# Kernel tuning notes

Measured on AMD Instinct MI355X. Metric: run time of the kernel, lower is better.

Reference implementation:

```python
import jax, jax.numpy as jnp
import numpy as np

HEAD_SIZE = 64


def setup_inputs() -> dict:
    key = jax.random.key(0)
    kx, kq, kk, kv = jax.random.split(key, 4)
    B, L, D = 4, 4096, 1024
    scale = 1.0 / np.sqrt(D)
    x = jax.random.normal(kx, (B, L, D), dtype=jnp.float32)
    Wq = jax.random.normal(kq, (D, HEAD_SIZE), dtype=jnp.float32) * scale
    Wk = jax.random.normal(kk, (D, HEAD_SIZE), dtype=jnp.float32) * scale
    Wv = jax.random.normal(kv, (D, HEAD_SIZE), dtype=jnp.float32) * scale
    return {"x": x, "Wq": Wq, "Wk": Wk, "Wv": Wv}


def reference(x, Wq, Wk, Wv):
    B, L, D = x.shape
    H = Wq.shape[1]
    q = jnp.einsum('bld,dh->blh', x, Wq)  # [B,L,H]
    k = jnp.einsum('bld,dh->blh', x, Wk)
    v = jnp.einsum('bld,dh->blh', x, Wv)
    # full L x L score matrix, as in the original module
    scores = jnp.einsum('bqh,bkh->bqk', q, k) / jnp.sqrt(jnp.float32(H))
    causal = jnp.tril(jnp.ones((L, L), dtype=bool))
    scores = jnp.where(causal, scores, -jnp.inf)
    attn = jax.nn.softmax(scores, axis=-1)
    z = jnp.einsum('bqk,bkh->bqh', attn, v)  # [B,L,H]
    return z
```

## Files before the change

kernel.cpp:

```cpp
#include <hip/hip_runtime.h>
#include <stdint.h>

#define L_SEQ 4096
#define D_MODEL 1024
#define HEAD 64
#define KCH 512
#define MAXCH 8
#define NQT 32

typedef unsigned short u16;
typedef _Float16 f16;
typedef __attribute__((ext_vector_type(8))) f16 f16x8;
typedef __attribute__((ext_vector_type(2))) __fp16 fp16x2;
typedef __attribute__((ext_vector_type(4))) float f32x4;

static __device__ __forceinline__ u16 f16bits(float f) {
    union { f16 h; u16 u; } c; c.h = (f16)f; return c.u;
}
static __device__ __forceinline__ uint32_t pk16(float a, float b) {
    union { fp16x2 h; uint32_t u; } c;
    c.h = __builtin_amdgcn_cvt_pkrtz(a, b);
    return c.u;
}
static __device__ __forceinline__ f16x8 ld8h(const u16* p) { return *(const f16x8*)p; }

static __device__ __forceinline__ f32x4 mfma16h(f16x8 a, f16x8 b, f32x4 c) {
    return __builtin_amdgcn_mfma_f32_16x16x32_f16(a, b, c, 0, 0, 0);
}

static __device__ __forceinline__ void gload16(const u16* g, u16* l) {
    __builtin_amdgcn_global_load_lds(
        (const __attribute__((address_space(1))) void*)g,
        (__attribute__((address_space(3))) void*)l, 16, 0, 0);
}

static __device__ __forceinline__ int Sq(int qt) {
    int f = qt >> 2, r = qt & 3;
    return (f + 1) * (2 * f + r);
}

__global__ __launch_bounds__(256) void conv_w(
    const float* __restrict__ Wq, const float* __restrict__ Wk,
    const float* __restrict__ Wv, u16* __restrict__ Wt)
{
    __shared__ u16 tile[64][72];
    const float* W = (blockIdx.y == 0) ? Wq : (blockIdx.y == 1) ? Wk : Wv;
    const float sc = (blockIdx.y == 0) ? 0.18033688f : 1.0f;
    u16* dst = Wt + blockIdx.y * (HEAD * D_MODEL);
    const int k0 = blockIdx.x * 64, t = threadIdx.x;
    #pragma unroll
    for (int i = 0; i < 16; i++) {
        int idx = i * 256 + t;
        int kk = idx >> 6, h = idx & 63;
        tile[h][kk] = f16bits(W[(size_t)(k0 + kk) * HEAD + h] * sc);
    }
    __syncthreads();
    #pragma unroll
    for (int i = 0; i < 16; i++) {
        int idx = i * 256 + t;
        int h = idx >> 6, kk = idx & 63;
        dst[(size_t)h * D_MODEL + k0 + kk] = tile[h][kk];
    }
}

__global__ __launch_bounds__(256, 4) void qkv_proj(
    const float* __restrict__ x, const u16* __restrict__ Wt,
    u16* __restrict__ qb, u16* __restrict__ kb, u16* __restrict__ vTb)
{
    __shared__ __align__(16) u16 Wl[2 * 192 * 32];
    __shared__ __align__(16) u16 Xl[2 * 32 * 36];
#define WLX(dh,r,c) Wl[((dh)*192 + (r))*32 + (c)]
#define XLX(kh,r,c) Xl[((kh)*32  + (r))*36 + (c)]
#define CT(r,c)     Wl[(r)*200 + (c)]

    const int t = threadIdx.x;
    const int wv = t >> 6, lane = t & 63;
    const int ln16 = lane & 15, quad = lane >> 4;
    const int w3 = wv * 3;
    const int m0 = blockIdx.x * 32;

    f32x4 acc[2][3] = {};
    float4 xv0, xv1;
    f16x8 wreg[6];

    auto loadW = [&](int s) {
        const int k0 = s * 64;
        #pragma unroll
        for (int k2 = 0; k2 < 6; k2++) {
            int c = wv * 6 + k2;
            int dh = c & 1, g = c >> 1;
            wreg[k2] = ld8h(Wt + (size_t)(g * 16 + (lane >> 2)) * D_MODEL
                               + k0 + dh * 32 + (lane & 3) * 8);
        }
    };
    auto writeW = [&]() {
        #pragma unroll
        for (int k2 = 0; k2 < 6; k2++) {
            int c = wv * 6 + k2;
            int dh = c & 1, g = c >> 1;
            *(f16x8*)&WLX(dh, g * 16 + (lane >> 2), (lane & 3) * 8) = wreg[k2];
        }
    };
    auto loadx = [&](int s) {
        const int k0 = s * 64;
        int r0 = t >> 4, cs0 = (t & 15) * 4;
        xv0 = *(const float4*)&x[(size_t)(m0 + r0) * D_MODEL + k0 + cs0];
        int idx = 256 + t, r1 = idx >> 4, cs1 = (idx & 15) * 4;
        xv1 = *(const float4*)&x[(size_t)(m0 + r1) * D_MODEL + k0 + cs1];
    };
    auto packx = [&]() {
        int r0 = t >> 4, cs0 = (t & 15) * 4;
        uint2 p0; p0.x = pk16(xv0.x, xv0.y); p0.y = pk16(xv0.z, xv0.w);
        *(uint2*)&XLX(cs0 >> 5, r0, cs0 & 31) = p0;
        int idx = 256 + t, r1 = idx >> 4, cs1 = (idx & 15) * 4;
        uint2 p1; p1.x = pk16(xv1.x, xv1.y); p1.y = pk16(xv1.z, xv1.w);
        *(uint2*)&XLX(cs1 >> 5, r1, cs1 & 31) = p1;
    };

    loadW(0); loadx(0); writeW(); packx();
    for (int s = 0; s < 16; s++) {
        __syncthreads();
        if (s + 1 < 16) { loadW(s + 1); loadx(s + 1); }
        #pragma unroll
        for (int c = 0; c < 2; c++) {
            f16x8 xb0 = ld8h(&XLX(c, ln16, quad * 8));
            f16x8 xb1 = ld8h(&XLX(c, 16 + ln16, quad * 8));
            #pragma unroll
            for (int j = 0; j < 3; j++) {
                f16x8 af = ld8h(&WLX(c, (w3 + j) * 16 + ln16, quad * 8));
                acc[0][j] = mfma16h(af, xb0, acc[0][j]);
                acc[1][j] = mfma16h(af, xb1, acc[1][j]);
            }
        }
        __syncthreads();
        if (s + 1 < 16) { writeW(); packx(); }
    }

    __syncthreads();
    #pragma unroll
    for (int mt = 0; mt < 2; mt++) {
        #pragma unroll
        for (int j = 0; j < 3; j++) {
            int g0 = (w3 + j) * 16 + quad * 4;
            uint2 pk;
            pk.x = pk16(acc[mt][j][0], acc[mt][j][1]);
            pk.y = pk16(acc[mt][j][2], acc[mt][j][3]);
            *(uint2*)&CT(mt * 16 + ln16, g0) = pk;
        }
    }
    __syncthreads();
    {
        int m = t >> 3, hg = (t & 7) * 8;
        *(f16x8*)&qb[(size_t)(m0 + m) * HEAD + hg] = *(f16x8*)&CT(m, hg);
        *(f16x8*)&kb[(size_t)(m0 + m) * HEAD + hg] = *(f16x8*)&CT(m, 64 + hg);
        int h = t >> 2, mg = (t & 3) * 8;
        f16x8 vvv;
        #pragma unroll
        for (int jj = 0; jj < 8; jj++)
            ((u16*)&vvv)[jj] = CT(mg + jj, 128 + h);
        int bbt = m0 >> 12, l0 = m0 & 4095;
        *(f16x8*)&vTb[(size_t)(bbt * HEAD + h) * L_SEQ + l0 + mg] = vvv;
    }
#undef WLX
#undef XLX
#undef CT
}

__global__ __launch_bounds__(256, 4) void attn_chunk(
    const u16* __restrict__ qb, const u16* __restrict__ kb,
    const u16* __restrict__ vT, float* __restrict__ Opart, float* __restrict__ lpart,
    float* __restrict__ out)
{
    const int id = blockIdx.x;
    const int b = id & 3;
    int qt, ch;
    if (id < 480) {
        int fi = id >> 2;
        int acc = 0;
        qt = 31; ch = 0;
        #pragma unroll
        for (int k = 0; k < 32; k++) {
            int nf = (k + 1) >> 2;
            if (fi < acc + nf) { qt = k; ch = fi - acc; break; }
            acc += nf;
        }
    } else {
        int pi = (id - 480) >> 2;
        int m = pi & 7;
        qt = (pi < 8) ? (4 * m + 2) : (pi < 16) ? (4 * m + 1) : (4 * m);
        ch = m;
    }

    __shared__ __align__(16) u16 Kls[2 * 64 * 32];
    __shared__ __align__(16) u16 Vls[2 * 64 * 32];
    __shared__ __align__(16) u16 Pls[4 * 32 * 72];
#define KBX(dh,r,c) Kls[((dh)*64 + (r))*32 + (c)]
#define VBX(kh,r,c) Vls[((kh)*64 + (r))*32 + (c)]
#define PX(r,c)     Pls[((wv)*32 + (r))*72 + (c)]

    const int t = threadIdx.x, wv = t >> 6, lane = t & 63;
    const int ln16 = lane & 15, quad = lane >> 4;
    const int qmin = qt * 128 + wv * 32;
    const int nch = (qt + 4) >> 2;

    f16x8 qf[2][2];
    #pragma unroll
    for (int qn = 0; qn < 2; qn++) {
        const u16* qrp = qb + (size_t)(b * L_SEQ + qmin + qn * 16 + ln16) * HEAD + quad * 8;
        qf[qn][0] = ld8h(qrp); qf[qn][1] = ld8h(qrp + 32);
    }

    const u16* kbb = kb + (size_t)b * L_SEQ * HEAD;
    const u16* vbb = vT + (size_t)b * HEAD * L_SEQ;

    f32x4 o[2][4] = {};
    float lsum[2] = {0.f, 0.f};

    const int kv_lo = ch * KCH;
    const int kv_hi = min(kv_lo + KCH, qt * 128 + 128);
    const int nst = (kv_hi - kv_lo) >> 6;

    auto issueK = [&](int kv0) {
        #pragma unroll
        for (int k2 = 0; k2 < 2; k2++) {
            int c = wv * 2 + k2;
            int dh = c & 1, g = c >> 1;
            const u16* gp = kbb + (size_t)(kv0 + g * 16 + (lane >> 2)) * HEAD
                                + dh * 32 + (lane & 3) * 8;
            gload16(gp, &KBX(dh, g * 16 + (lane >> 2), (lane & 3) * 8));
        }
    };
    auto issueV = [&](int kv0) {
        #pragma unroll
        for (int k2 = 0; k2 < 2; k2++) {
            int c = wv * 2 + k2;
            int kh = c & 1, g = c >> 1;
            const u16* gp = vbb + (size_t)(g * 16 + (lane >> 2)) * L_SEQ
                                + kv0 + kh * 32 + (lane & 3) * 8;
            gload16(gp, &VBX(kh, g * 16 + (lane >> 2), (lane & 3) * 8));
        }
    };

    issueK(kv_lo); issueV(kv_lo);
    __syncthreads();

    for (int s = 0; s < nst; s++) {
        const int kv0 = kv_lo + s * 64;

        #pragma unroll
        for (int g = 0; g < 4; g++) {
            f16x8 ka0 = ld8h(&KBX(0, g * 16 + ln16, quad * 8));
            f16x8 ka1 = ld8h(&KBX(1, g * 16 + ln16, quad * 8));
            #pragma unroll
            for (int qn = 0; qn < 2; qn++) {
                f32x4 s2 = {};
                s2 = mfma16h(ka0, qf[qn][0], s2);
                s2 = mfma16h(ka1, qf[qn][1], s2);
                float p0, p1, p2, p3;
                if (kv0 + g * 16 + 15 <= qmin + qn * 16) {
                    p0 = __builtin_amdgcn_exp2f(s2[0]);
                    p1 = __builtin_amdgcn_exp2f(s2[1]);
                    p2 = __builtin_amdgcn_exp2f(s2[2]);
                    p3 = __builtin_amdgcn_exp2f(s2[3]);
                } else {
                    int q = qmin + qn * 16 + ln16;
                    int kv = kv0 + g * 16 + quad * 4;
                    p0 = (kv     <= q) ? __builtin_amdgcn_exp2f(s2[0]) : 0.f;
                    p1 = (kv + 1 <= q) ? __builtin_amdgcn_exp2f(s2[1]) : 0.f;
                    p2 = (kv + 2 <= q) ? __builtin_amdgcn_exp2f(s2[2]) : 0.f;
                    p3 = (kv + 3 <= q) ? __builtin_amdgcn_exp2f(s2[3]) : 0.f;
                }
                lsum[qn] += (p0 + p1) + (p2 + p3);
                uint2 pk; pk.x = pk16(p0, p1); pk.y = pk16(p2, p3);
                *(uint2*)&PX(qn * 16 + ln16, g * 16 + quad * 4) = pk;
            }
        }

        __syncthreads();
        if (s + 1 < nst) issueK(kv0 + 64);

        f16x8 pf[2][2];
        #pragma unroll
        for (int qn = 0; qn < 2; qn++) {
            pf[qn][0] = ld8h(&PX(qn * 16 + ln16, quad * 8));
            pf[qn][1] = ld8h(&PX(qn * 16 + ln16, 32 + quad * 8));
        }
        #pragma unroll
        for (int hg = 0; hg < 4; hg++) {
            f16x8 va0 = ld8h(&VBX(0, hg * 16 + ln16, quad * 8));
            f16x8 va1 = ld8h(&VBX(1, hg * 16 + ln16, quad * 8));
            #pragma unroll
            for (int qn = 0; qn < 2; qn++) {
                o[qn][hg] = mfma16h(va0, pf[qn][0], o[qn][hg]);
                o[qn][hg] = mfma16h(va1, pf[qn][1], o[qn][hg]);
            }
        }

        __syncthreads();
        if (s + 1 < nst) issueV(kv0 + 64);
    }

    #pragma unroll
    for (int qn = 0; qn < 2; qn++) {
        lsum[qn] += __shfl_xor(lsum[qn], 16);
        lsum[qn] += __shfl_xor(lsum[qn], 32);
    }

    if (nch == 1) {
        #pragma unroll
        for (int qn = 0; qn < 2; qn++) {
            float inv = 1.f / lsum[qn];
            int q = qmin + qn * 16 + ln16;
            #pragma unroll
            for (int hg = 0; hg < 4; hg++) {
                float4 r;
                r.x = o[qn][hg][0] * inv; r.y = o[qn][hg][1] * inv;
                r.z = o[qn][hg][2] * inv; r.w = o[qn][hg][3] * inv;
                *(float4*)&out[((size_t)(b * L_SEQ + q)) * HEAD + hg * 16 + quad * 4] = r;
            }
        }
        return;
    }

    const size_t base = (size_t)(b * 144 + Sq(qt) + ch);
    #pragma unroll
    for (int qn = 0; qn < 2; qn++) {
        int q_local = wv * 32 + qn * 16 + ln16;
        #pragma unroll
        for (int hg = 0; hg < 4; hg++)
            *(f32x4*)&Opart[base * 8192 + (size_t)q_local * 64 + hg * 16 + quad * 4] = o[qn][hg];
        if (quad == 0)
            lpart[base * 128 + q_local] = lsum[qn];
    }
#undef KBX
#undef VBX
#undef PX
}

__global__ __launch_bounds__(256) void merge_chunks(
    const float* __restrict__ Opart, const float* __restrict__ lpart,
    float* __restrict__ out)
{
    const int qt = blockIdx.x + 4, qseg = blockIdx.y, b = blockIdx.z;
    const int nch = (qt + 4) >> 2;
    const int t = threadIdx.x;
    const size_t obase = (size_t)(b * 144 + Sq(qt)) * 8192;
    const size_t lbase = (size_t)(b * 144 + Sq(qt)) * 128;
    #pragma unroll
    for (int i = 0; i < 2; i++) {
        int idx = i * 256 + t;
        int q = qseg * 32 + (idx >> 4), hg = (idx & 15) * 4;
        float L = 0.f, ax = 0.f, ay = 0.f, az = 0.f, aw = 0.f;
        #pragma unroll
        for (int c = 0; c < MAXCH; c++) {
            if (c < nch) {
                L += lpart[lbase + c * 128 + q];
                const float4 v = *(const float4*)&Opart[obase + (size_t)c * 8192 + q * 64 + hg];
                ax += v.x; ay += v.y; az += v.z; aw += v.w;
            }
        }
        float inv = 1.f / L;
        float4 r; r.x = ax * inv; r.y = ay * inv; r.z = az * inv; r.w = aw * inv;
        *(float4*)&out[((size_t)(b * L_SEQ + qt * 128 + q)) * HEAD + hg] = r;
    }
}

extern "C" void kernel_launch(void* const* d_in, const int* in_sizes, int n_in,
                              void* d_out, int out_size, void* d_ws, size_t ws_size,
                              hipStream_t stream) {
    const float* x  = (const float*)d_in[0];
    const float* Wq = (const float*)d_in[1];
    const float* Wk = (const float*)d_in[2];
    const float* Wv = (const float*)d_in[3];
    float* out = (float*)d_out;

    u16* ws16 = (u16*)d_ws;
    u16* Wt  = ws16;
    u16* qb  = Wt + 3 * HEAD * D_MODEL;
    u16* kb  = qb + 16384 * HEAD;
    u16* vTb = kb + 16384 * HEAD;
    float* Opart = (float*)(vTb + 16384 * HEAD);
    float* lpart = Opart + (size_t)4 * 144 * 8192;

    conv_w      <<<dim3(16, 3), 256, 0, stream>>>(Wq, Wk, Wv, Wt);
    qkv_proj    <<<dim3(512), 256, 0, stream>>>(x, Wt, qb, kb, vTb);
    attn_chunk  <<<dim3(576), 256, 0, stream>>>(qb, kb, vTb, Opart, lpart, out);
    merge_chunks<<<dim3(NQT - 4, 4, 4), 256, 0, stream>>>(Opart, lpart, out);
}
```

Before: 146.9 us.

## XOR-swizzle shared-memory tiles and double-buffer x prefetch two stages ahead

Applies an XOR swizzle to the 16-byte column chunks of the W, K and V shared-memory tiles, in both the projection and the attention kernels. This is meant to cut LDS bank conflicts on the row-strided MFMA operand reads. For K/V the swizzle is applied on the global-load address side of the direct-to-LDS loads. The projection kernel also keeps two sets of x registers and prefetches x two stages ahead so global latency is better hidden, at the cost of extra VGPRs.

```diff
diff --git a/kernel.cpp b/kernel.cpp
--- a/kernel.cpp
+++ b/kernel.cpp
@@ -78,9 +78,12 @@
     const int ln16 = lane & 15, quad = lane >> 4;
     const int w3 = wv * 3;
     const int m0 = blockIdx.x * 32;
+    const int r4 = lane >> 2, cl = lane & 3;
+    const int cswz = (cl ^ (r4 & 3)) * 8;
+    const int qsw = (quad ^ (ln16 & 3)) * 8;
 
     f32x4 acc[2][3] = {};
-    float4 xv0, xv1;
+    float4 xa0, xa1, xb0, xb1;
     f16x8 wreg[6];
 
     auto loadW = [&](int s) {
@@ -89,8 +92,8 @@
         for (int k2 = 0; k2 < 6; k2++) {
             int c = wv * 6 + k2;
             int dh = c & 1, g = c >> 1;
-            wreg[k2] = ld8h(Wt + (size_t)(g * 16 + (lane >> 2)) * D_MODEL
-                               + k0 + dh * 32 + (lane & 3) * 8);
+            wreg[k2] = ld8h(Wt + (size_t)(g * 16 + r4) * D_MODEL
+                               + k0 + dh * 32 + cl * 8);
         }
     };
     auto writeW = [&]() {
@@ -98,42 +101,62 @@
         for (int k2 = 0; k2 < 6; k2++) {
             int c = wv * 6 + k2;
             int dh = c & 1, g = c >> 1;
-            *(f16x8*)&WLX(dh, g * 16 + (lane >> 2), (lane & 3) * 8) = wreg[k2];
-        }
-    };
-    auto loadx = [&](int s) {
+            *(f16x8*)&WLX(dh, g * 16 + r4, cswz) = wreg[k2];
+        }
+    };
+    auto loadxAB = [&](int s, float4& v0, float4& v1) {
         const int k0 = s * 64;
-        int r0 = t >> 4, cs0 = (t & 15) * 4;
-        xv0 = *(const float4*)&x[(size_t)(m0 + r0) * D_MODEL + k0 + cs0];
-        int idx = 256 + t, r1 = idx >> 4, cs1 = (idx & 15) * 4;
-        xv1 = *(const float4*)&x[(size_t)(m0 + r1) * D_MODEL + k0 + cs1];
-    };
-    auto packx = [&]() {
-        int r0 = t >> 4, cs0 = (t & 15) * 4;
-        uint2 p0; p0.x = pk16(xv0.x, xv0.y); p0.y = pk16(xv0.z, xv0.w);
-        *(uint2*)&XLX(cs0 >> 5, r0, cs0 & 31) = p0;
-        int idx = 256 + t, r1 = idx >> 4, cs1 = (idx & 15) * 4;
-        uint2 p1; p1.x = pk16(xv1.x, xv1.y); p1.y = pk16(xv1.z, xv1.w);
-        *(uint2*)&XLX(cs1 >> 5, r1, cs1 & 31) = p1;
-    };
-
-    loadW(0); loadx(0); writeW(); packx();
-    for (int s = 0; s < 16; s++) {
-        __syncthreads();
-        if (s + 1 < 16) { loadW(s + 1); loadx(s + 1); }
+        int rr0 = t >> 4, cs0 = (t & 15) * 4;
+        v0 = *(const float4*)&x[(size_t)(m0 + rr0) * D_MODEL + k0 + cs0];
+        int idx = 256 + t, rr1 = idx >> 4, cs1 = (idx & 15) * 4;
+        v1 = *(const float4*)&x[(size_t)(m0 + rr1) * D_MODEL + k0 + cs1];
+    };
+    auto packxAB = [&](const float4& v0, const float4& v1) {
+        int rr0 = t >> 4, cs0 = (t & 15) * 4;
+        uint2 p0; p0.x = pk16(v0.x, v0.y); p0.y = pk16(v0.z, v0.w);
+        *(uint2*)&XLX(cs0 >> 5, rr0, cs0 & 31) = p0;
+        int idx = 256 + t, rr1 = idx >> 4, cs1 = (idx & 15) * 4;
+        uint2 p1; p1.x = pk16(v1.x, v1.y); p1.y = pk16(v1.z, v1.w);
+        *(uint2*)&XLX(cs1 >> 5, rr1, cs1 & 31) = p1;
+    };
+    auto mfmaBody = [&]() {
         #pragma unroll
         for (int c = 0; c < 2; c++) {
-            f16x8 xb0 = ld8h(&XLX(c, ln16, quad * 8));
-            f16x8 xb1 = ld8h(&XLX(c, 16 + ln16, quad * 8));
+            f16x8 xb_0 = ld8h(&XLX(c, ln16, quad * 8));
+            f16x8 xb_1 = ld8h(&XLX(c, 16 + ln16, quad * 8));
             #pragma unroll
             for (int j = 0; j < 3; j++) {
-                f16x8 af = ld8h(&WLX(c, (w3 + j) * 16 + ln16, quad * 8));
-                acc[0][j] = mfma16h(af, xb0, acc[0][j]);
-                acc[1][j] = mfma16h(af, xb1, acc[1][j]);
+                f16x8 af = ld8h(&WLX(c, (w3 + j) * 16 + ln16, qsw));
+                acc[0][j] = mfma16h(af, xb_0, acc[0][j]);
+                acc[1][j] = mfma16h(af, xb_1, acc[1][j]);
             }
         }
-        __syncthreads();
-        if (s + 1 < 16) { writeW(); packx(); }
+    };
+
+    loadW(0); loadxAB(0, xa0, xa1);
+    writeW(); packxAB(xa0, xa1);
+    loadxAB(1, xb0, xb1);
+
+    #pragma unroll 1
+    for (int sp = 0; sp < 8; sp++) {
+        {
+            int s = 2 * sp;
+            __syncthreads();
+            if (s + 1 < 16) loadW(s + 1);
+            if (s + 2 < 16) loadxAB(s + 2, xa0, xa1);
+            mfmaBody();
+            __syncthreads();
+            if (s + 1 < 16) { writeW(); packxAB(xb0, xb1); }
+        }
+        {
+            int s = 2 * sp + 1;
+            __syncthreads();
+            if (s + 1 < 16) loadW(s + 1);
+            if (s + 2 < 16) loadxAB(s + 2, xb0, xb1);
+            mfmaBody();
+            __syncthreads();
+            if (s + 1 < 16) { writeW(); packxAB(xa0, xa1); }
+        }
     }
 
     __syncthreads();
@@ -202,6 +225,9 @@
     const int ln16 = lane & 15, quad = lane >> 4;
     const int qmin = qt * 128 + wv * 32;
     const int nch = (qt + 4) >> 2;
+    const int r4 = lane >> 2, cl = lane & 3;
+    const int csw8 = ((cl ^ (r4 & 3))) * 8;
+    const int qsw = (quad ^ (ln16 & 3)) * 8;
 
     f16x8 qf[2][2];
     #pragma unroll
@@ -225,9 +251,9 @@
         for (int k2 = 0; k2 < 2; k2++) {
             int c = wv * 2 + k2;
             int dh = c & 1, g = c >> 1;
-            const u16* gp = kbb + (size_t)(kv0 + g * 16 + (lane >> 2)) * HEAD
-                                + dh * 32 + (lane & 3) * 8;
-            gload16(gp, &KBX(dh, g * 16 + (lane >> 2), (lane & 3) * 8));
+            const u16* gp = kbb + (size_t)(kv0 + g * 16 + r4) * HEAD
+                                + dh * 32 + csw8;
+            gload16(gp, &KBX(dh, g * 16 + r4, cl * 8));
         }
     };
     auto issueV = [&](int kv0) {
@@ -235,9 +261,9 @@
         for (int k2 = 0; k2 < 2; k2++) {
             int c = wv * 2 + k2;
             int kh = c & 1, g = c >> 1;
-            const u16* gp = vbb + (size_t)(g * 16 + (lane >> 2)) * L_SEQ
-                                + kv0 + kh * 32 + (lane & 3) * 8;
-            gload16(gp, &VBX(kh, g * 16 + (lane >> 2), (lane & 3) * 8));
+            const u16* gp = vbb + (size_t)(g * 16 + r4) * L_SEQ
+                                + kv0 + kh * 32 + csw8;
+            gload16(gp, &VBX(kh, g * 16 + r4, cl * 8));
         }
     };
 
@@ -249,8 +275,8 @@
 
         #pragma unroll
         for (int g = 0; g < 4; g++) {
-            f16x8 ka0 = ld8h(&KBX(0, g * 16 + ln16, quad * 8));
-            f16x8 ka1 = ld8h(&KBX(1, g * 16 + ln16, quad * 8));
+            f16x8 ka0 = ld8h(&KBX(0, g * 16 + ln16, qsw));
+            f16x8 ka1 = ld8h(&KBX(1, g * 16 + ln16, qsw));
             #pragma unroll
             for (int qn = 0; qn < 2; qn++) {
                 f32x4 s2 = {};
@@ -287,8 +313,8 @@
         }
         #pragma unroll
         for (int hg = 0; hg < 4; hg++) {
-            f16x8 va0 = ld8h(&VBX(0, hg * 16 + ln16, quad * 8));
-            f16x8 va1 = ld8h(&VBX(1, hg * 16 + ln16, quad * 8));
+            f16x8 va0 = ld8h(&VBX(0, hg * 16 + ln16, qsw));
+            f16x8 va1 = ld8h(&VBX(1, hg * 16 + ln16, qsw));
             #pragma unroll
             for (int qn = 0; qn < 2; qn++) {
                 o[qn][hg] = mfma16h(va0, pf[qn][0], o[qn][hg]);
```

Result: no change. 147.6 us (+0.5%).

## Double K-step tile depth in projection and attention kernels to halve barriers

Applied to the files above, without the earlier changes.

The QKV projection now stages 128 reduction columns of W and x per iteration instead of 64, so it runs 8 iterations instead of 16. The attention kernel now loads 128 keys/values per stage and processes them as two 64-wide halves, computing the first half's PV product before the barrier. The aim is to cut the number of block barriers and loop iterations and to give more independent work between global loads. In exchange, LDS use and register use roughly double, so launch bounds drop to 2 blocks per CU for the projection and 3 for attention, which lowers occupancy.

```diff
diff --git a/kernel.cpp b/kernel.cpp
--- a/kernel.cpp
+++ b/kernel.cpp
@@ -63,12 +63,12 @@
     }
 }
 
-__global__ __launch_bounds__(256, 4) void qkv_proj(
+__global__ __launch_bounds__(256, 2) void qkv_proj(
     const float* __restrict__ x, const u16* __restrict__ Wt,
     u16* __restrict__ qb, u16* __restrict__ kb, u16* __restrict__ vTb)
 {
-    __shared__ __align__(16) u16 Wl[2 * 192 * 32];
-    __shared__ __align__(16) u16 Xl[2 * 32 * 36];
+    __shared__ __align__(16) u16 Wl[4 * 192 * 32];
+    __shared__ __align__(16) u16 Xl[4 * 32 * 36];
 #define WLX(dh,r,c) Wl[((dh)*192 + (r))*32 + (c)]
 #define XLX(kh,r,c) Xl[((kh)*32  + (r))*36 + (c)]
 #define CT(r,c)     Wl[(r)*200 + (c)]
@@ -78,51 +78,59 @@
     const int ln16 = lane & 15, quad = lane >> 4;
     const int w3 = wv * 3;
     const int m0 = blockIdx.x * 32;
+    const int r4 = lane >> 2, cl8 = (lane & 3) * 8;
 
     f32x4 acc[2][3] = {};
-    float4 xv0, xv1;
-    f16x8 wreg[6];
+    float4 xv0, xv1, xv2, xv3;
+    f16x8 wreg[12];
 
     auto loadW = [&](int s) {
-        const int k0 = s * 64;
-        #pragma unroll
-        for (int k2 = 0; k2 < 6; k2++) {
-            int c = wv * 6 + k2;
-            int dh = c & 1, g = c >> 1;
-            wreg[k2] = ld8h(Wt + (size_t)(g * 16 + (lane >> 2)) * D_MODEL
-                               + k0 + dh * 32 + (lane & 3) * 8);
+        const int k0 = s * 128;
+        #pragma unroll
+        for (int k2 = 0; k2 < 12; k2++) {
+            int c = wv * 12 + k2;
+            int dh = c & 3, g = c >> 2;
+            wreg[k2] = ld8h(Wt + (size_t)(g * 16 + r4) * D_MODEL
+                               + k0 + dh * 32 + cl8);
         }
     };
     auto writeW = [&]() {
         #pragma unroll
-        for (int k2 = 0; k2 < 6; k2++) {
-            int c = wv * 6 + k2;
-            int dh = c & 1, g = c >> 1;
-            *(f16x8*)&WLX(dh, g * 16 + (lane >> 2), (lane & 3) * 8) = wreg[k2];
-        }
-    };
+        for (int k2 = 0; k2 < 12; k2++) {
+            int c = wv * 12 + k2;
+            int dh = c & 3, g = c >> 2;
+            *(f16x8*)&WLX(dh, g * 16 + r4, cl8) = wreg[k2];
+        }
+    };
+    const int xc4 = (t & 31) * 4;
+    const int xr0 = t >> 5;
     auto loadx = [&](int s) {
-        const int k0 = s * 64;
-        int r0 = t >> 4, cs0 = (t & 15) * 4;
-        xv0 = *(const float4*)&x[(size_t)(m0 + r0) * D_MODEL + k0 + cs0];
-        int idx = 256 + t, r1 = idx >> 4, cs1 = (idx & 15) * 4;
-        xv1 = *(const float4*)&x[(size_t)(m0 + r1) * D_MODEL + k0 + cs1];
+        const int k0 = s * 128;
+        const float* xp = &x[(size_t)(m0 + xr0) * D_MODEL + k0 + xc4];
+        xv0 = *(const float4*)(xp);
+        xv1 = *(const float4*)(xp +  8 * D_MODEL);
+        xv2 = *(const float4*)(xp + 16 * D_MODEL);
+        xv3 = *(const float4*)(xp + 24 * D_MODEL);
     };
     auto packx = [&]() {
-        int r0 = t >> 4, cs0 = (t & 15) * 4;
-        uint2 p0; p0.x = pk16(xv0.x, xv0.y); p0.y = pk16(xv0.z, xv0.w);
-        *(uint2*)&XLX(cs0 >> 5, r0, cs0 & 31) = p0;
-        int idx = 256 + t, r1 = idx >> 4, cs1 = (idx & 15) * 4;
-        uint2 p1; p1.x = pk16(xv1.x, xv1.y); p1.y = pk16(xv1.z, xv1.w);
-        *(uint2*)&XLX(cs1 >> 5, r1, cs1 & 31) = p1;
+        const int kh = xc4 >> 5, ci = xc4 & 31;
+        uint2 p;
+        p.x = pk16(xv0.x, xv0.y); p.y = pk16(xv0.z, xv0.w);
+        *(uint2*)&XLX(kh, xr0,      ci) = p;
+        p.x = pk16(xv1.x, xv1.y); p.y = pk16(xv1.z, xv1.w);
+        *(uint2*)&XLX(kh, xr0 +  8, ci) = p;
+        p.x = pk16(xv2.x, xv2.y); p.y = pk16(xv2.z, xv2.w);
+        *(uint2*)&XLX(kh, xr0 + 16, ci) = p;
+        p.x = pk16(xv3.x, xv3.y); p.y = pk16(xv3.z, xv3.w);
+        *(uint2*)&XLX(kh, xr0 + 24, ci) = p;
     };
 
     loadW(0); loadx(0); writeW(); packx();
-    for (int s = 0; s < 16; s++) {
+    for (int s = 0; s < 8; s++) {
         __syncthreads();
-        if (s + 1 < 16) { loadW(s + 1); loadx(s + 1); }
-        #pragma unroll
-        for (int c = 0; c < 2; c++) {
+        if (s + 1 < 8) { loadW(s + 1); loadx(s + 1); }
+        #pragma unroll
+        for (int c = 0; c < 4; c++) {
             f16x8 xb0 = ld8h(&XLX(c, ln16, quad * 8));
             f16x8 xb1 = ld8h(&XLX(c, 16 + ln16, quad * 8));
             #pragma unroll
@@ -133,7 +141,7 @@
             }
         }
         __syncthreads();
-        if (s + 1 < 16) { writeW(); packx(); }
+        if (s + 1 < 8) { writeW(); packx(); }
     }
 
     __syncthreads();
@@ -166,7 +174,7 @@
 #undef CT
 }
 
-__global__ __launch_bounds__(256, 4) void attn_chunk(
+__global__ __launch_bounds__(256, 3) void attn_chunk(
     const u16* __restrict__ qb, const u16* __restrict__ kb,
     const u16* __restrict__ vT, float* __restrict__ Opart, float* __restrict__ lpart,
     float* __restrict__ out)
@@ -191,17 +199,18 @@
         ch = m;
     }
 
-    __shared__ __align__(16) u16 Kls[2 * 64 * 32];
-    __shared__ __align__(16) u16 Vls[2 * 64 * 32];
+    __shared__ __align__(16) u16 Kls[4 * 64 * 32];
+    __shared__ __align__(16) u16 Vls[4 * 64 * 32];
     __shared__ __align__(16) u16 Pls[4 * 32 * 72];
-#define KBX(dh,r,c) Kls[((dh)*64 + (r))*32 + (c)]
-#define VBX(kh,r,c) Vls[((kh)*64 + (r))*32 + (c)]
-#define PX(r,c)     Pls[((wv)*32 + (r))*72 + (c)]
+#define KBX(hf,dh,r,c) Kls[((((hf)*2+(dh))*64) + (r))*32 + (c)]
+#define VBX(hf,kh,r,c) Vls[((((hf)*2+(kh))*64) + (r))*32 + (c)]
+#define PX(r,c)        Pls[((wv)*32 + (r))*72 + (c)]
 
     const int t = threadIdx.x, wv = t >> 6, lane = t & 63;
     const int ln16 = lane & 15, quad = lane >> 4;
     const int qmin = qt * 128 + wv * 32;
     const int nch = (qt + 4) >> 2;
+    const int r4 = lane >> 2, cl8 = (lane & 3) * 8;
 
     f16x8 qf[2][2];
     #pragma unroll
@@ -218,53 +227,48 @@
 
     const int kv_lo = ch * KCH;
     const int kv_hi = min(kv_lo + KCH, qt * 128 + 128);
-    const int nst = (kv_hi - kv_lo) >> 6;
+    const int nst = (kv_hi - kv_lo) >> 7;
 
     auto issueK = [&](int kv0) {
         #pragma unroll
-        for (int k2 = 0; k2 < 2; k2++) {
-            int c = wv * 2 + k2;
-            int dh = c & 1, g = c >> 1;
-            const u16* gp = kbb + (size_t)(kv0 + g * 16 + (lane >> 2)) * HEAD
-                                + dh * 32 + (lane & 3) * 8;
-            gload16(gp, &KBX(dh, g * 16 + (lane >> 2), (lane & 3) * 8));
+        for (int k2 = 0; k2 < 4; k2++) {
+            int c = wv * 4 + k2;
+            int dh = c & 1, g = (c >> 1) & 3, hf = c >> 3;
+            const u16* gp = kbb + (size_t)(kv0 + hf * 64 + g * 16 + r4) * HEAD
+                                + dh * 32 + cl8;
+            gload16(gp, &KBX(hf, dh, g * 16 + r4, cl8));
         }
     };
     auto issueV = [&](int kv0) {
         #pragma unroll
-        for (int k2 = 0; k2 < 2; k2++) {
-            int c = wv * 2 + k2;
-            int kh = c & 1, g = c >> 1;
-            const u16* gp = vbb + (size_t)(g * 16 + (lane >> 2)) * L_SEQ
-                                + kv0 + kh * 32 + (lane & 3) * 8;
-            gload16(gp, &VBX(kh, g * 16 + (lane >> 2), (lane & 3) * 8));
-        }
-    };
-
-    issueK(kv_lo); issueV(kv_lo);
-    __syncthreads();
-
-    for (int s = 0; s < nst; s++) {
-        const int kv0 = kv_lo + s * 64;
-
+        for (int k2 = 0; k2 < 4; k2++) {
+            int c = wv * 4 + k2;
+            int kh = c & 1, g = (c >> 1) & 3, hf = c >> 3;
+            const u16* gp = vbb + (size_t)(g * 16 + r4) * L_SEQ
+                                + kv0 + hf * 64 + kh * 32 + cl8;
+            gload16(gp, &VBX(hf, kh, g * 16 + r4, cl8));
+        }
+    };
+
+    auto qk_half = [&](int hf, int kv0h) {
         #pragma unroll
         for (int g = 0; g < 4; g++) {
-            f16x8 ka0 = ld8h(&KBX(0, g * 16 + ln16, quad * 8));
-            f16x8 ka1 = ld8h(&KBX(1, g * 16 + ln16, quad * 8));
+            f16x8 ka0 = ld8h(&KBX(hf, 0, g * 16 + ln16, quad * 8));
+            f16x8 ka1 = ld8h(&KBX(hf, 1, g * 16 + ln16, quad * 8));
             #pragma unroll
             for (int qn = 0; qn < 2; qn++) {
                 f32x4 s2 = {};
                 s2 = mfma16h(ka0, qf[qn][0], s2);
                 s2 = mfma16h(ka1, qf[qn][1], s2);
                 float p0, p1, p2, p3;
-                if (kv0 + g * 16 + 15 <= qmin + qn * 16) {
+                if (kv0h + g * 16 + 15 <= qmin + qn * 16) {
                     p0 = __builtin_amdgcn_exp2f(s2[0]);
                     p1 = __builtin_amdgcn_exp2f(s2[1]);
                     p2 = __builtin_amdgcn_exp2f(s2[2]);
                     p3 = __builtin_amdgcn_exp2f(s2[3]);
                 } else {
                     int q = qmin + qn * 16 + ln16;
-                    int kv = kv0 + g * 16 + quad * 4;
+                    int kv = kv0h + g * 16 + quad * 4;
                     p0 = (kv     <= q) ? __builtin_amdgcn_exp2f(s2[0]) : 0.f;
                     p1 = (kv + 1 <= q) ? __builtin_amdgcn_exp2f(s2[1]) : 0.f;
                     p2 = (kv + 2 <= q) ? __builtin_amdgcn_exp2f(s2[2]) : 0.f;
@@ -275,10 +279,8 @@
                 *(uint2*)&PX(qn * 16 + ln16, g * 16 + quad * 4) = pk;
             }
         }
-
-        __syncthreads();
-        if (s + 1 < nst) issueK(kv0 + 64);
-
+    };
+    auto pv_half = [&](int hf) {
         f16x8 pf[2][2];
         #pragma unroll
         for (int qn = 0; qn < 2; qn++) {
@@ -287,17 +289,33 @@
         }
         #pragma unroll
         for (int hg = 0; hg < 4; hg++) {
-            f16x8 va0 = ld8h(&VBX(0, hg * 16 + ln16, quad * 8));
-            f16x8 va1 = ld8h(&VBX(1, hg * 16 + ln16, quad * 8));
+            f16x8 va0 = ld8h(&VBX(hf, 0, hg * 16 + ln16, quad * 8));
+            f16x8 va1 = ld8h(&VBX(hf, 1, hg * 16 + ln16, quad * 8));
             #pragma unroll
             for (int qn = 0; qn < 2; qn++) {
                 o[qn][hg] = mfma16h(va0, pf[qn][0], o[qn][hg]);
                 o[qn][hg] = mfma16h(va1, pf[qn][1], o[qn][hg]);
             }
         }
+    };
+
+    issueK(kv_lo); issueV(kv_lo);
+    __syncthreads();
+
+    for (int s = 0; s < nst; s++) {
+        const int kv0 = kv_lo + s * 128;
+
+        qk_half(0, kv0);
+        pv_half(0);
+        qk_half(1, kv0 + 64);
 
         __syncthreads();
-        if (s + 1 < nst) issueV(kv0 + 64);
+        if (s + 1 < nst) issueK(kv0 + 128);
+
+        pv_half(1);
+
+        __syncthreads();
+        if (s + 1 < nst) issueV(kv0 + 128);
     }
 
     #pragma unroll
```

Result: no change. 144.0 us (-1.9%).
